# Kernel optimization log

Hardware: AMD Instinct MI355X
Metric: run time of the kernel (lower is better)

## Reference

```python
import jax, jax.numpy as jnp
import numpy as np

B, C, K, HH, WW, D = 2, 4, 32, 96, 96, 64


def setup_inputs() -> dict:
    key = jax.random.key(0)
    k1, k2, k3, k4, k5 = jax.random.split(key, 5)
    heatmaps = jax.random.uniform(k1, (B, C, K, HH, WW), dtype=jnp.float32)
    # Projection matrices: random linear part, translation column centered at
    # (H/2, W/2, 1) so that most cube points project inside the heatmap with z>0.
    P = 5.0 * jax.random.normal(k2, (B, C, 3, 4), dtype=jnp.float32)
    center = jnp.array([HH / 2.0, WW / 2.0, 1.0], dtype=jnp.float32)
    P = P.at[:, :, :, 3].set(center + 0.1 * jax.random.normal(k3, (B, C, 3)))
    coord_cubes = jax.random.uniform(k4, (B, D, D, D, 3), dtype=jnp.float32,
                                     minval=-1.0, maxval=1.0)
    vol_confidences = jax.random.uniform(k5, (B, C, K), dtype=jnp.float32) + 0.1
    return {
        "heatmaps": heatmaps,
        "projection_matrices": P,
        "coord_cubes": coord_cubes,
        "vol_confidences": vol_confidences,
    }


def _unproject(heatmaps, P, coord_cubes, conf):
    """Vectorized port of `unprojection` with agg_type='conf'.

    heatmaps: (B,C,K,H,W); P: (B,C,3,4); coord_cubes: (B,D,D,D,3); conf: (B,C,K)
    Returns volumes (B,K,D,D,D).
    """
    b, c, k, H, W = heatmaps.shape
    d = coord_cubes.shape[1]
    n = d * d * d
    coords = coord_cubes.reshape(b, n, 3)
    homo = jnp.concatenate([coords, jnp.ones((b, n, 1), coords.dtype)], axis=-1)
    # Projective transform per camera: (B,C,N,3)
    proj = jnp.einsum('bnj,bcij->bcni', homo, P)
    z = proj[..., 2]
    invalid = z <= 0.0
    z_safe = jnp.where(z == 0.0, 1.0, z)
    u = proj[..., 0] / z_safe
    v = proj[..., 1] / z_safe
    # Normalization exactly as in the source (x divided by H, y by W)
    gx = 2.0 * (u / H - 0.5)
    gy = 2.0 * (v / W - 0.5)
    # grid_sample align_corners=True: x indexes width, y indexes height
    ix = (gx + 1.0) * 0.5 * (W - 1)
    iy = (gy + 1.0) * 0.5 * (H - 1)
    x0 = jnp.floor(ix)
    y0 = jnp.floor(iy)
    x1 = x0 + 1.0
    y1 = y0 + 1.0
    wx1 = ix - x0
    wx0 = 1.0 - wx1
    wy1 = iy - y0
    wy0 = 1.0 - wy1
    hm = heatmaps.reshape(b, c, k, H * W)

    def corner(xc, yc, w):
        inb = (xc >= 0) & (xc <= W - 1) & (yc >= 0) & (yc <= H - 1)
        xi = jnp.clip(xc, 0, W - 1).astype(jnp.int32)
        yi = jnp.clip(yc, 0, H - 1).astype(jnp.int32)
        idx = (yi * W + xi)[:, :, None, :]                  # (B,C,1,N)
        idx = jnp.broadcast_to(idx, (b, c, k, idx.shape[-1]))
        g = jnp.take_along_axis(hm, idx, axis=3)            # (B,C,K,N)
        return g * (w * inb)[:, :, None, :]

    val = (corner(x0, y0, wx0 * wy0) + corner(x1, y0, wx1 * wy0)
           + corner(x0, y1, wx0 * wy1) + corner(x1, y1, wx1 * wy1))
    val = jnp.where(invalid[:, :, None, :], 0.0, val)       # zero invalid voxels
    # 'conf' aggregation; confidences normalized over cameras as in forward()
    conf_n = conf / conf.sum(axis=1, keepdims=True)
    vol = (val * conf_n[..., None]).sum(axis=1)             # (B,K,N)
    return vol.reshape(b, k, d, d, d)


def reference(heatmaps, projection_matrices, coord_cubes, vol_confidences):
    return _unproject(heatmaps, projection_matrices, coord_cubes, vol_confidences)
```

## Files before the change

### kernel.cpp

```cpp
#include <hip/hip_runtime.h>
#include <hip/hip_bf16.h>

#define BB 2
#define CC 4
#define KK 32
#define HHH 96
#define WWW 96
#define DDD 64
#define NN (DDD * DDD * DDD)
#define HWSZ (HHH * WWW)

__global__ __launch_bounds__(256) void hm_transpose(const float* __restrict__ in,
                                                    float* __restrict__ out) {
  __shared__ float tile[KK][64 + 1];
  const int bc  = blockIdx.y;
  const int hw0 = blockIdx.x * 64;
  const int t   = threadIdx.x;

  const float* src = in + (size_t)bc * KK * HWSZ;
  const int lhw = t & 63, lk0 = t >> 6;
#pragma unroll
  for (int i = 0; i < 8; ++i) {
    const int k = lk0 + i * 4;
    tile[k][lhw] = src[(size_t)k * HWSZ + hw0 + lhw];
  }
  __syncthreads();

  float* dst = out + ((size_t)bc * HWSZ + hw0) * KK;
  const int lk = t & 31, lh0 = t >> 5;
#pragma unroll
  for (int i = 0; i < 8; ++i) {
    const int h = lh0 + i * 8;
    dst[(size_t)h * KK + lk] = tile[lk][h];
  }
}

__global__ __launch_bounds__(256) void unproject2(
    const float* __restrict__ hmT,
    const float* __restrict__ Pm,
    const float* __restrict__ coords,
    const float* __restrict__ conf,
    float* __restrict__ out) {
  __shared__ float sP[CC * 12];
  __shared__ float sConf[CC][KK];
  __shared__ float sXYZ[32 * 3];
  __shared__ float vtile[32][KK + 1];

  const int t     = threadIdx.x;
  const int vbase = blockIdx.x * 32;
  const int b     = vbase >> 18;
  const int nbase = vbase & (NN - 1);

  if (t < CC * 12) sP[t] = Pm[b * CC * 12 + t];
  if (t < 96)      sXYZ[t] = coords[(size_t)vbase * 3 + t];
  if (t < KK) {
    const float c0 = conf[(b * CC + 0) * KK + t];
    const float c1 = conf[(b * CC + 1) * KK + t];
    const float c2 = conf[(b * CC + 2) * KK + t];
    const float c3 = conf[(b * CC + 3) * KK + t];
    const float s  = c0 + c1 + c2 + c3;
    sConf[0][t] = c0 / s;
    sConf[1][t] = c1 / s;
    sConf[2][t] = c2 / s;
    sConf[3][t] = c3 / s;
  }
  __syncthreads();

  const int v = t >> 3;
  const int j = t & 7;
  const float x = sXYZ[v * 3 + 0];
  const float y = sXYZ[v * 3 + 1];
  const float z = sXYZ[v * 3 + 2];

  float4 acc = make_float4(0.f, 0.f, 0.f, 0.f);

  const float sxc = (float)(WWW - 1) / (float)HHH;
  const float syc = (float)(HHH - 1) / (float)WWW;

#pragma unroll
  for (int c = 0; c < CC; ++c) {
    const float* P = &sP[c * 12];
    const float pz = P[8] * x + P[9] * y + P[10] * z + P[11];
    if (pz > 0.0f) {
      const float px = P[0] * x + P[1] * y + P[2] * z + P[3];
      const float py = P[4] * x + P[5] * y + P[6] * z + P[7];
      const float u = px / pz, v2 = py / pz;
      const float ix = u * sxc, iy = v2 * syc;
      const float x0f = floorf(ix), y0f = floorf(iy);
      const float x1f = x0f + 1.0f, y1f = y0f + 1.0f;
      const float wx1 = ix - x0f, wx0 = 1.0f - wx1;
      const float wy1 = iy - y0f, wy0 = 1.0f - wy1;
      const float ibx0 = (x0f >= 0.f && x0f <= (float)(WWW - 1)) ? 1.f : 0.f;
      const float ibx1 = (x1f >= 0.f && x1f <= (float)(WWW - 1)) ? 1.f : 0.f;
      const float iby0 = (y0f >= 0.f && y0f <= (float)(HHH - 1)) ? 1.f : 0.f;
      const float iby1 = (y1f >= 0.f && y1f <= (float)(HHH - 1)) ? 1.f : 0.f;
      const float w00 = wx0 * wy0 * ibx0 * iby0;
      const float w01 = wx1 * wy0 * ibx1 * iby0;
      const float w10 = wx0 * wy1 * ibx0 * iby1;
      const float w11 = wx1 * wy1 * ibx1 * iby1;
      const int x0i = (int)fminf(fmaxf(x0f, 0.f), (float)(WWW - 1));
      const int x1i = (int)fminf(fmaxf(x1f, 0.f), (float)(WWW - 1));
      const int y0i = (int)fminf(fmaxf(y0f, 0.f), (float)(HHH - 1));
      const int y1i = (int)fminf(fmaxf(y1f, 0.f), (float)(HHH - 1));

      const float* base = hmT + (size_t)(b * CC + c) * HWSZ * KK + j * 4;
      const float4 g00 = *(const float4*)(base + (y0i * WWW + x0i) * KK);
      const float4 g01 = *(const float4*)(base + (y0i * WWW + x1i) * KK);
      const float4 g10 = *(const float4*)(base + (y1i * WWW + x0i) * KK);
      const float4 g11 = *(const float4*)(base + (y1i * WWW + x1i) * KK);
      const float4 w   = ((const float4*)sConf[c])[j];
      acc.x += (g00.x * w00 + g01.x * w01 + g10.x * w10 + g11.x * w11) * w.x;
      acc.y += (g00.y * w00 + g01.y * w01 + g10.y * w10 + g11.y * w11) * w.y;
      acc.z += (g00.z * w00 + g01.z * w01 + g10.z * w10 + g11.z * w11) * w.z;
      acc.w += (g00.w * w00 + g01.w * w01 + g10.w * w10 + g11.w * w11) * w.w;
    }
  }

  vtile[v][j * 4 + 0] = acc.x;
  vtile[v][j * 4 + 1] = acc.y;
  vtile[v][j * 4 + 2] = acc.z;
  vtile[v][j * 4 + 3] = acc.w;
  __syncthreads();

  float* ob = out + (size_t)b * KK * NN + nbase;
#pragma unroll
  for (int q = 0; q < 4; ++q) {
    const int idx = t + q * 256;
    const int k   = idx >> 5;
    const int n0  = idx & 31;
    ob[(size_t)k * NN + n0] = vtile[n0][k];
  }
}

__global__ __launch_bounds__(256) void unproject_native(
    const float* __restrict__ hm, const float* __restrict__ Pm,
    const float* __restrict__ coords, const float* __restrict__ conf,
    float* __restrict__ out) {
  __shared__ float sP[CC * 12];
  __shared__ float sConf[CC * KK];
  const int t   = threadIdx.x;
  const int gid = blockIdx.x * 256 + t;
  const int b   = gid >> 18;
  const int n   = gid & (NN - 1);
  if (t < CC * 12) sP[t] = Pm[b * CC * 12 + t];
  if (t < KK) {
    const float c0 = conf[(b * CC + 0) * KK + t];
    const float c1 = conf[(b * CC + 1) * KK + t];
    const float c2 = conf[(b * CC + 2) * KK + t];
    const float c3 = conf[(b * CC + 3) * KK + t];
    const float s  = c0 + c1 + c2 + c3;
    sConf[0 * KK + t] = c0 / s; sConf[1 * KK + t] = c1 / s;
    sConf[2 * KK + t] = c2 / s; sConf[3 * KK + t] = c3 / s;
  }
  __syncthreads();
  const float x = coords[(size_t)gid * 3 + 0];
  const float y = coords[(size_t)gid * 3 + 1];
  const float z = coords[(size_t)gid * 3 + 2];
  float accs[KK];
#pragma unroll
  for (int k = 0; k < KK; ++k) accs[k] = 0.f;
  const float sxc = (float)(WWW - 1) / (float)HHH;
  const float syc = (float)(HHH - 1) / (float)WWW;
#pragma unroll
  for (int c = 0; c < CC; ++c) {
    const float* P = &sP[c * 12];
    const float pz = P[8] * x + P[9] * y + P[10] * z + P[11];
    if (pz > 0.0f) {
      const float px = P[0] * x + P[1] * y + P[2] * z + P[3];
      const float py = P[4] * x + P[5] * y + P[6] * z + P[7];
      const float u = px / pz, v2 = py / pz;
      const float ix = u * sxc, iy = v2 * syc;
      const float x0f = floorf(ix), y0f = floorf(iy);
      const float x1f = x0f + 1.0f, y1f = y0f + 1.0f;
      const float wx1 = ix - x0f, wx0 = 1.0f - wx1;
      const float wy1 = iy - y0f, wy0 = 1.0f - wy1;
      const float ibx0 = (x0f >= 0.f && x0f <= (float)(WWW - 1)) ? 1.f : 0.f;
      const float ibx1 = (x1f >= 0.f && x1f <= (float)(WWW - 1)) ? 1.f : 0.f;
      const float iby0 = (y0f >= 0.f && y0f <= (float)(HHH - 1)) ? 1.f : 0.f;
      const float iby1 = (y1f >= 0.f && y1f <= (float)(HHH - 1)) ? 1.f : 0.f;
      const float w00 = wx0 * wy0 * ibx0 * iby0;
      const float w01 = wx1 * wy0 * ibx1 * iby0;
      const float w10 = wx0 * wy1 * ibx0 * iby1;
      const float w11 = wx1 * wy1 * ibx1 * iby1;
      const int x0i = (int)fminf(fmaxf(x0f, 0.f), (float)(WWW - 1));
      const int x1i = (int)fminf(fmaxf(x1f, 0.f), (float)(WWW - 1));
      const int y0i = (int)fminf(fmaxf(y0f, 0.f), (float)(HHH - 1));
      const int y1i = (int)fminf(fmaxf(y1f, 0.f), (float)(HHH - 1));
      const float* bse = hm + (size_t)(b * CC + c) * KK * HWSZ;
      const int i00 = y0i * WWW + x0i, i01 = y0i * WWW + x1i;
      const int i10 = y1i * WWW + x0i, i11 = y1i * WWW + x1i;
#pragma unroll
      for (int k = 0; k < KK; ++k) {
        const float* hk = bse + (size_t)k * HWSZ;
        accs[k] += (hk[i00] * w00 + hk[i01] * w01 +
                    hk[i10] * w10 + hk[i11] * w11) * sConf[c * KK + k];
      }
    }
  }
  float* ob = out + (size_t)b * KK * NN + n;
#pragma unroll
  for (int k = 0; k < KK; ++k) ob[(size_t)k * NN] = accs[k];
}

extern "C" void kernel_launch(void* const* d_in, const int* in_sizes, int n_in,
                              void* d_out, int out_size, void* d_ws, size_t ws_size,
                              hipStream_t stream) {
  const float* heatmaps = (const float*)d_in[0];
  const float* Pm       = (const float*)d_in[1];
  const float* coords   = (const float*)d_in[2];
  const float* conf     = (const float*)d_in[3];
  float* out            = (float*)d_out;

  const size_t hmT_bytes = (size_t)BB * CC * HWSZ * KK * sizeof(float);

  if (ws_size >= hmT_bytes) {
    float* hmT = (float*)d_ws;
    dim3 tg(HWSZ / 64, BB * CC);
    hm_transpose<<<tg, 256, 0, stream>>>(heatmaps, hmT);
    const int grid = (BB * NN) / 32;
    unproject2<<<grid, 256, 0, stream>>>(hmT, Pm, coords, conf, out);
  } else {
    const int grid = (BB * NN) / 256;
    unproject_native<<<grid, 256, 0, stream>>>(heatmaps, Pm, coords, conf, out);
  }
}
```

Before: 129.5 us.

## Precompute per-voxel projection once into LDS and process 256 voxels per block

Result: faster. 122.0 us (-5.7%).

```diff
diff --git a/kernel.cpp b/kernel.cpp
--- a/kernel.cpp
+++ b/kernel.cpp
@@ -35,24 +35,24 @@
   }
 }
 
-__global__ __launch_bounds__(256) void unproject2(
+__global__ __launch_bounds__(256) void unproject3(
     const float* __restrict__ hmT,
     const float* __restrict__ Pm,
     const float* __restrict__ coords,
     const float* __restrict__ conf,
     float* __restrict__ out) {
-  __shared__ float sP[CC * 12];
-  __shared__ float sConf[CC][KK];
-  __shared__ float sXYZ[32 * 3];
-  __shared__ float vtile[32][KK + 1];
+  __shared__ float  sP[CC * 12];
+  __shared__ float  sConf[CC][KK];
+  __shared__ int4   sOff[CC][256];
+  __shared__ float4 sW[CC][256];
+  __shared__ float  vtile[32][KK + 1];
 
   const int t     = threadIdx.x;
-  const int vbase = blockIdx.x * 32;
+  const int vbase = blockIdx.x * 256;
   const int b     = vbase >> 18;
   const int nbase = vbase & (NN - 1);
 
   if (t < CC * 12) sP[t] = Pm[b * CC * 12 + t];
-  if (t < 96)      sXYZ[t] = coords[(size_t)vbase * 3 + t];
   if (t < KK) {
     const float c0 = conf[(b * CC + 0) * KK + t];
     const float c1 = conf[(b * CC + 1) * KK + t];
@@ -66,25 +66,21 @@
   }
   __syncthreads();
 
-  const int v = t >> 3;
-  const int j = t & 7;
-  const float x = sXYZ[v * 3 + 0];
-  const float y = sXYZ[v * 3 + 1];
-  const float z = sXYZ[v * 3 + 2];
-
-  float4 acc = make_float4(0.f, 0.f, 0.f, 0.f);
-
-  const float sxc = (float)(WWW - 1) / (float)HHH;
-  const float syc = (float)(HHH - 1) / (float)WWW;
-
-#pragma unroll
-  for (int c = 0; c < CC; ++c) {
-    const float* P = &sP[c * 12];
-    const float pz = P[8] * x + P[9] * y + P[10] * z + P[11];
-    if (pz > 0.0f) {
+  {
+    const float x = coords[(size_t)(vbase + t) * 3 + 0];
+    const float y = coords[(size_t)(vbase + t) * 3 + 1];
+    const float z = coords[(size_t)(vbase + t) * 3 + 2];
+    const float sxc = (float)(WWW - 1) / (float)HHH;
+    const float syc = (float)(HHH - 1) / (float)WWW;
+#pragma unroll
+    for (int c = 0; c < CC; ++c) {
+      const float* P = &sP[c * 12];
+      const float pz = P[8] * x + P[9] * y + P[10] * z + P[11];
+      const float valid = (pz > 0.0f) ? 1.0f : 0.0f;
+      const float zs    = (pz > 0.0f) ? pz : 1.0f;
       const float px = P[0] * x + P[1] * y + P[2] * z + P[3];
       const float py = P[4] * x + P[5] * y + P[6] * z + P[7];
-      const float u = px / pz, v2 = py / pz;
+      const float u = px / zs, v2 = py / zs;
       const float ix = u * sxc, iy = v2 * syc;
       const float x0f = floorf(ix), y0f = floorf(iy);
       const float x1f = x0f + 1.0f, y1f = y0f + 1.0f;
@@ -94,41 +90,62 @@
       const float ibx1 = (x1f >= 0.f && x1f <= (float)(WWW - 1)) ? 1.f : 0.f;
       const float iby0 = (y0f >= 0.f && y0f <= (float)(HHH - 1)) ? 1.f : 0.f;
       const float iby1 = (y1f >= 0.f && y1f <= (float)(HHH - 1)) ? 1.f : 0.f;
-      const float w00 = wx0 * wy0 * ibx0 * iby0;
-      const float w01 = wx1 * wy0 * ibx1 * iby0;
-      const float w10 = wx0 * wy1 * ibx0 * iby1;
-      const float w11 = wx1 * wy1 * ibx1 * iby1;
       const int x0i = (int)fminf(fmaxf(x0f, 0.f), (float)(WWW - 1));
       const int x1i = (int)fminf(fmaxf(x1f, 0.f), (float)(WWW - 1));
       const int y0i = (int)fminf(fmaxf(y0f, 0.f), (float)(HHH - 1));
       const int y1i = (int)fminf(fmaxf(y1f, 0.f), (float)(HHH - 1));
-
-      const float* base = hmT + (size_t)(b * CC + c) * HWSZ * KK + j * 4;
-      const float4 g00 = *(const float4*)(base + (y0i * WWW + x0i) * KK);
-      const float4 g01 = *(const float4*)(base + (y0i * WWW + x1i) * KK);
-      const float4 g10 = *(const float4*)(base + (y1i * WWW + x0i) * KK);
-      const float4 g11 = *(const float4*)(base + (y1i * WWW + x1i) * KK);
-      const float4 w   = ((const float4*)sConf[c])[j];
-      acc.x += (g00.x * w00 + g01.x * w01 + g10.x * w10 + g11.x * w11) * w.x;
-      acc.y += (g00.y * w00 + g01.y * w01 + g10.y * w10 + g11.y * w11) * w.y;
-      acc.z += (g00.z * w00 + g01.z * w01 + g10.z * w10 + g11.z * w11) * w.z;
-      acc.w += (g00.w * w00 + g01.w * w01 + g10.w * w10 + g11.w * w11) * w.w;
-    }
-  }
-
-  vtile[v][j * 4 + 0] = acc.x;
-  vtile[v][j * 4 + 1] = acc.y;
-  vtile[v][j * 4 + 2] = acc.z;
-  vtile[v][j * 4 + 3] = acc.w;
-  __syncthreads();
-
+      sOff[c][t] = make_int4(y0i * WWW + x0i, y0i * WWW + x1i,
+                             y1i * WWW + x0i, y1i * WWW + x1i);
+      sW[c][t] = make_float4(wx0 * wy0 * (ibx0 * iby0 * valid),
+                             wx1 * wy0 * (ibx1 * iby0 * valid),
+                             wx0 * wy1 * (ibx0 * iby1 * valid),
+                             wx1 * wy1 * (ibx1 * iby1 * valid));
+    }
+  }
+  __syncthreads();
+
+  const int vloc = t >> 3;
+  const int j    = t & 7;
+
+  float4 cf[CC];
+#pragma unroll
+  for (int c = 0; c < CC; ++c) cf[c] = ((const float4*)sConf[c])[j];
+
+  const float* base0 = hmT + (size_t)b * CC * HWSZ * KK + j * 4;
   float* ob = out + (size_t)b * KK * NN + nbase;
-#pragma unroll
-  for (int q = 0; q < 4; ++q) {
-    const int idx = t + q * 256;
-    const int k   = idx >> 5;
-    const int n0  = idx & 31;
-    ob[(size_t)k * NN + n0] = vtile[n0][k];
+
+  for (int pass = 0; pass < 8; ++pass) {
+    const int v = pass * 32 + vloc;
+    float4 acc = make_float4(0.f, 0.f, 0.f, 0.f);
+#pragma unroll
+    for (int c = 0; c < CC; ++c) {
+      const float4 w = sW[c][v];
+      if (w.x + w.y + w.z + w.w > 0.0f) {
+        const int4 off = sOff[c][v];
+        const float* bc = base0 + (size_t)c * HWSZ * KK;
+        const float4 g00 = *(const float4*)(bc + (size_t)off.x * KK);
+        const float4 g01 = *(const float4*)(bc + (size_t)off.y * KK);
+        const float4 g10 = *(const float4*)(bc + (size_t)off.z * KK);
+        const float4 g11 = *(const float4*)(bc + (size_t)off.w * KK);
+        acc.x += (g00.x * w.x + g01.x * w.y + g10.x * w.z + g11.x * w.w) * cf[c].x;
+        acc.y += (g00.y * w.x + g01.y * w.y + g10.y * w.z + g11.y * w.w) * cf[c].y;
+        acc.z += (g00.z * w.x + g01.z * w.y + g10.z * w.z + g11.z * w.w) * cf[c].z;
+        acc.w += (g00.w * w.x + g01.w * w.y + g10.w * w.z + g11.w * w.w) * cf[c].w;
+      }
+    }
+    vtile[vloc][j * 4 + 0] = acc.x;
+    vtile[vloc][j * 4 + 1] = acc.y;
+    vtile[vloc][j * 4 + 2] = acc.z;
+    vtile[vloc][j * 4 + 3] = acc.w;
+    __syncthreads();
+#pragma unroll
+    for (int q = 0; q < 4; ++q) {
+      const int idx = t + q * 256;
+      const int k   = idx >> 5;
+      const int n0  = idx & 31;
+      ob[(size_t)k * NN + pass * 32 + n0] = vtile[n0][k];
+    }
+    __syncthreads();
   }
 }
 
@@ -217,8 +234,8 @@
     float* hmT = (float*)d_ws;
     dim3 tg(HWSZ / 64, BB * CC);
     hm_transpose<<<tg, 256, 0, stream>>>(heatmaps, hmT);
-    const int grid = (BB * NN) / 32;
-    unproject2<<<grid, 256, 0, stream>>>(hmT, Pm, coords, conf, out);
+    const int grid = (BB * NN) / 256;
+    unproject3<<<grid, 256, 0, stream>>>(hmT, Pm, coords, conf, out);
   } else {
     const int grid = (BB * NN) / 256;
     unproject_native<<<grid, 256, 0, stream>>>(heatmaps, Pm, coords, conf, out);
```
